# Optimization experiments

Hardware: AMD Instinct MI355X
Metric: run time of the kernel (lower is better)

The kernel has to match this reference:

```python
import jax, jax.numpy as jnp
import numpy as np

B, D, CTX, H = 8192, 64, 256, 512  # batch, latent dim (made.nin), context dim, MADE hidden


def _masks(D, H):
    """Standard MADE natural-ordering masks (Germain et al. 2015)."""
    m0 = np.arange(1, D + 1)                 # input degrees 1..D
    mh = (np.arange(H) % (D - 1)) + 1        # hidden degrees 1..D-1
    M1 = (mh[:, None] >= m0[None, :]).astype(np.float32)   # (H, D)
    M2 = (mh[:, None] >= mh[None, :]).astype(np.float32)   # (H, H)
    mo = np.concatenate([m0, m0])            # outputs = [means; pre_scales]
    Mo = (mo[:, None] > mh[None, :]).astype(np.float32)    # (2D, H)
    return jnp.asarray(M1), jnp.asarray(M2), jnp.asarray(Mo)


def setup_inputs() -> dict:
    key = jax.random.key(0)
    ks = jax.random.split(key, 7)
    s = 0.05
    return {
        "context": jax.random.normal(ks[0], (B, CTX), jnp.float32),
        "eps": jax.random.normal(ks[1], (B, D), jnp.float32),  # reparameterization noise
        "W1": jax.random.normal(ks[2], (H, D), jnp.float32) * s,
        "b1": jnp.zeros((H,), jnp.float32),
        "Wc": jax.random.normal(ks[3], (H, CTX), jnp.float32) * s,
        "W2": jax.random.normal(ks[4], (H, H), jnp.float32) * s,
        "b2": jnp.zeros((H,), jnp.float32),
        "Wo": jax.random.normal(ks[5], (2 * D, H), jnp.float32) * s,
        "bo": jnp.zeros((2 * D,), jnp.float32),
    }


def reference(context, eps, W1, b1, Wc, W2, b2, Wo, bo):
    """AutoRegressiveDistribution.rsample (gaussian): D sequential MADE forwards,
    each extracting column i of (mu, softplus(pre_scale)) and sampling z_i."""
    M1, M2, Mo = _masks(D, H)
    W1m, W2m, Wom = (W1 * M1).T, (W2 * M2).T, (Wo * Mo).T
    ctx_h = context @ Wc.T  # context projection is constant across steps

    def step(z, i):
        h = jax.nn.relu(z @ W1m + ctx_h + b1)   # (B, H)
        h = jax.nn.relu(h @ W2m + b2)           # (B, H)
        out = h @ Wom + bo                      # (B, 2D): [means | pre_scales]
        mu_i = out[:, i]
        scale_i = jax.nn.softplus(out[:, D + i])
        z_i = mu_i + scale_i * eps[:, i]        # Normal(mu, scale).rsample()
        z = z.at[:, i].set(z_i)
        return z, (mu_i, scale_i)

    z0 = jnp.zeros((context.shape[0], D), context.dtype)
    z, (mus, scales) = jax.lax.scan(step, z0, jnp.arange(D))
    # state = (z_sample, mu_inferred, scale_inferred), each (B, D)
    return z, mus.T, scales.T
```

## Files before the change

kernel.cpp:

```cpp
#include <hip/hip_runtime.h>
#include <math.h>


typedef float f2 __attribute__((ext_vector_type(2)));

#define Bn 8192
#define Dn 64
#define CTXn 256
#define Hn 512
#define On 128
#define Rn 8

#define WQ_SZ  (64 * 512 * 12)
#define WOQ_SZ (64 * 64 * 20)
#define WCP_SZ (CTXn * Hn)

__device__ __forceinline__ int perm_of(int p, int* degout) {
  int k, t;
  if (p < 72) { k = p / 9 + 1; t = p - (k - 1) * 9; }
  else        { int pp = p - 72; k = pp / 8 + 9; t = pp - (k - 9) * 8; }
  *degout = k;
  return (k - 1) + 63 * t;
}
__device__ __forceinline__ int inv_perm(int h) {
  int i = h % 63;
  int t = h / 63;
  int base = (i < 9) ? 9 * i : 72 + 8 * (i - 8);
  return base + t;
}

#define R0e 262144
#define R1e (R0e + 32768)
#define R2e (R1e + 65536)
#define R3e (R2e + 131072)
#define R4e (R3e + 35840)
#define R5e (R4e + 1024)
__global__ void prep_kernel(const float* __restrict__ W1, const float* __restrict__ Wc,
                            const float* __restrict__ W2, const float* __restrict__ Wo,
                            const float* __restrict__ b1, const float* __restrict__ b2,
                            float* __restrict__ Wq, float* __restrict__ Woq,
                            float* __restrict__ WcpT, float* __restrict__ b1p,
                            float* __restrict__ b2p) {
  int idx = blockIdx.x * 256 + threadIdx.x;
  if (idx < R0e) {
    int hq = idx >> 9, hp = idx & 511;
    int i = hp % 63, e = hp / 63;
    Wq[i * 6144 + inv_perm(hq) * 12 + e] = W2[idx];
  } else if (idx < R1e) {
    int jj = idx - R0e;
    int hq = jj >> 6, i = jj & 63;
    Wq[i * 6144 + inv_perm(hq) * 12 + 9] = W1[jj];
  } else if (idx < R2e) {
    int jj = idx - R1e;
    int o = jj >> 9, hp = jj & 511;
    int i = hp % 63, p = hp / 63;
    int j = o & 63, half = o >> 6;
    Woq[i * 1280 + j * 20 + half * 10 + p] = Wo[jj];
  } else if (idx < R3e) {
    int jj = idx - R2e;
    int hq = jj >> 8, cc = jj & 255;
    WcpT[cc * 512 + inv_perm(hq)] = Wc[jj];
  } else if (idx < R4e) {
    int z = idx - R3e;
    if (z < 28672) {
      int i = 8 + (z >> 9), q = z & 511;
      Wq[i * 6144 + q * 12 + 8] = 0.f;
    } else {
      int z2 = z - 28672;
      int i = 8 + (z2 >> 7), r = z2 & 127;
      int j = r & 63, half = r >> 6;
      Woq[i * 1280 + j * 20 + half * 10 + 8] = 0.f;
    }
  } else if (idx < R5e) {
    int z = idx - R4e;
    if (z < 512) {
      int dq; int hq = perm_of(z, &dq);
      b1p[z] = b1[hq];
    } else {
      int q = z - 512;
      int dq; int hq = perm_of(q, &dq);
      b2p[q] = b2[hq];
    }
  }
}

__global__ __launch_bounds__(256, 4)
void made_pk_kernel(
    const float* __restrict__ context, const float* __restrict__ WcpT,
    const float* __restrict__ b1p,
    const float* __restrict__ Wq, const float* __restrict__ Woq,
    const float* __restrict__ b2p, const float* __restrict__ bo,
    const float* __restrict__ eps, float* __restrict__ out) {
  __shared__ __align__(16) float ctxR[8][264];
  __shared__ __align__(16) float zcur[8];
  __shared__ __align__(16) float h1g[9][8];
  __shared__ __align__(16) float h2g[9][8];

  int t = threadIdx.x;
  int b0 = blockIdx.x * Rn;
  int rp = t >> 6, l = t & 63;
  int q0 = t, q1 = t + 256;

  int g0 = ((q0 < 72) ? q0 / 9 + 1 : (q0 - 72) / 8 + 9) - 1;
  int g1 = ((q1 - 72) / 8 + 9) - 1;
  int qm = t | 63;
  int gm0s = __builtin_amdgcn_readfirstlane(
      ((qm < 72) ? qm / 9 + 1 : (qm - 72) / 8 + 9) - 1);
  int gm1s = __builtin_amdgcn_readfirstlane(((qm + 256 - 72) / 8 + 9) - 1);

  #pragma unroll
  for (int r = 0; r < 8; ++r)
    ctxR[r][t] = context[(b0 + r) * CTXn + t];
  __syncthreads();

  float acc0[8], acc1[8];
  {
    float bias0 = b1p[q0], bias1 = b1p[q1];
    #pragma unroll
    for (int r = 0; r < 8; ++r) { acc0[r] = bias0; acc1[r] = bias1; }
  }
  {
    const float* wc = WcpT;
    #pragma clang loop unroll(disable)
    for (int c4 = 0; c4 < CTXn / 4; ++c4) {
      float xr[8][4];
      #pragma unroll
      for (int r = 0; r < 8; ++r) {
        float4 x = *(const float4*)&ctxR[r][4 * c4];
        xr[r][0] = x.x; xr[r][1] = x.y; xr[r][2] = x.z; xr[r][3] = x.w;
      }
      #pragma unroll
      for (int k = 0; k < 4; ++k) {
        float w0 = wc[q0], w1 = wc[q1];
        #pragma unroll
        for (int r = 0; r < 8; ++r) {
          acc0[r] = fmaf(xr[r][k], w0, acc0[r]);
          acc1[r] = fmaf(xr[r][k], w1, acc1[r]);
        }
        wc += Hn;
      }
    }
  }

  f2 a10[4], a11[4], a20[4], a21[4];
  #pragma unroll
  for (int r2 = 0; r2 < 4; ++r2) {
    a10[r2] = (f2){acc0[2 * r2], acc0[2 * r2 + 1]};
    a11[r2] = (f2){acc1[2 * r2], acc1[2 * r2 + 1]};
  }
  {
    float bb0 = b2p[q0], bb1 = b2p[q1];
    #pragma unroll
    for (int r2 = 0; r2 < 4; ++r2) {
      a20[r2] = (f2){bb0, bb0};
      a21[r2] = (f2){bb1, bb1};
    }
  }
  f2 ocA = (f2){bo[l], bo[l]};
  f2 ocB = (f2){bo[l + 64], bo[l + 64]};
  f2 ez2 = (f2){eps[(b0 + 2 * rp) * Dn + l], eps[(b0 + 2 * rp + 1) * Dn + l]};
  f2 zs = (f2){0.f, 0.f}, mus = zs, scs = zs;

  const float* wq0p = Wq + (size_t)q0 * 12;
  const float* wq1p = Wq + (size_t)q1 * 12;
  const float* wopp = Woq + (size_t)l * 20;

  #pragma clang loop unroll(disable)
  for (int i = 0; i < Dn; ++i) {
    if (l == i) {
      f2 pre = ocB;
      float sx = fmaxf(pre.x, 0.f) + __logf(1.f + __expf(-fabsf(pre.x)));
      float sy = fmaxf(pre.y, 0.f) + __logf(1.f + __expf(-fabsf(pre.y)));
      f2 sc = (f2){sx, sy};
      f2 z = ocA + sc * ez2;
      *(f2*)&zcur[2 * rp] = z;
      zs = z; mus = ocA; scs = sc;
    }
    __syncthreads();

    int sb = (i < 8) ? 9 * i : 8 * i + 8;
    bool liveB = (i <= gm1s);
    bool liveA = (i <= gm0s);
    float4 A1c0, A1c1, A1c2, A0c0, A0c1, A0c2;
    if (liveB) {
      const float4* a4 = (const float4*)wq1p;
      A1c0 = a4[0]; A1c1 = a4[1]; A1c2 = a4[2];
      if (liveA) {
        const float4* b4 = (const float4*)wq0p;
        A0c0 = b4[0]; A0c1 = b4[1]; A0c2 = b4[2];
      }
      float4 za = *(const float4*)&zcur[0];
      float4 zb = *(const float4*)&zcur[4];
      f2 zc0 = (f2){za.x, za.y}, zc1 = (f2){za.z, za.w};
      f2 zc2 = (f2){zb.x, zb.y}, zc3 = (f2){zb.z, zb.w};
      {
        f2 wv = (f2){A1c2.y, A1c2.y};
        a11[0] += wv * zc0; a11[1] += wv * zc1;
        a11[2] += wv * zc2; a11[3] += wv * zc3;
        if (g1 == i) {
          int pp = q1 - sb;
          float4 h0 = {fmaxf(a11[0].x, 0.f), fmaxf(a11[0].y, 0.f),
                       fmaxf(a11[1].x, 0.f), fmaxf(a11[1].y, 0.f)};
          float4 h1_ = {fmaxf(a11[2].x, 0.f), fmaxf(a11[2].y, 0.f),
                        fmaxf(a11[3].x, 0.f), fmaxf(a11[3].y, 0.f)};
          *(float4*)&h1g[pp][0] = h0; *(float4*)&h1g[pp][4] = h1_;
        }
      }
      if (liveA) {
        f2 wv = (f2){A0c2.y, A0c2.y};
        a10[0] += wv * zc0; a10[1] += wv * zc1;
        a10[2] += wv * zc2; a10[3] += wv * zc3;
        if (g0 == i) {
          int pp = q0 - sb;
          float4 h0 = {fmaxf(a10[0].x, 0.f), fmaxf(a10[0].y, 0.f),
                       fmaxf(a10[1].x, 0.f), fmaxf(a10[1].y, 0.f)};
          float4 h1_ = {fmaxf(a10[2].x, 0.f), fmaxf(a10[2].y, 0.f),
                        fmaxf(a10[3].x, 0.f), fmaxf(a10[3].y, 0.f)};
          *(float4*)&h1g[pp][0] = h0; *(float4*)&h1g[pp][4] = h1_;
        }
      }
    }
    __syncthreads();

    const float4* w4 = (const float4*)wopp;
    float4 B0 = w4[0], B1 = w4[1], B2 = w4[2], B3 = w4[3], B4 = w4[4];

    if (liveB) {
      float wA1[9] = {A1c0.x, A1c0.y, A1c0.z, A1c0.w,
                      A1c1.x, A1c1.y, A1c1.z, A1c1.w, A1c2.x};
      if (liveA) {
        float wA0[9] = {A0c0.x, A0c0.y, A0c0.z, A0c0.w,
                        A0c1.x, A0c1.y, A0c1.z, A0c1.w, A0c2.x};
        #pragma unroll
        for (int p = 0; p < 9; ++p) {
          float4 ha = *(const float4*)&h1g[p][0];
          float4 hb = *(const float4*)&h1g[p][4];
          f2 h0 = (f2){ha.x, ha.y}, h1_ = (f2){ha.z, ha.w};
          f2 h2_ = (f2){hb.x, hb.y}, h3 = (f2){hb.z, hb.w};
          f2 wv1 = (f2){wA1[p], wA1[p]};
          f2 wv0 = (f2){wA0[p], wA0[p]};
          a21[0] += wv1 * h0; a21[1] += wv1 * h1_;
          a21[2] += wv1 * h2_; a21[3] += wv1 * h3;
          a20[0] += wv0 * h0; a20[1] += wv0 * h1_;
          a20[2] += wv0 * h2_; a20[3] += wv0 * h3;
        }
      } else {
        #pragma unroll
        for (int p = 0; p < 9; ++p) {
          float4 ha = *(const float4*)&h1g[p][0];
          float4 hb = *(const float4*)&h1g[p][4];
          f2 h0 = (f2){ha.x, ha.y}, h1_ = (f2){ha.z, ha.w};
          f2 h2_ = (f2){hb.x, hb.y}, h3 = (f2){hb.z, hb.w};
          f2 wv1 = (f2){wA1[p], wA1[p]};
          a21[0] += wv1 * h0; a21[1] += wv1 * h1_;
          a21[2] += wv1 * h2_; a21[3] += wv1 * h3;
        }
      }
      if (g1 == i) {
        int pp = q1 - sb;
        float4 h0 = {fmaxf(a21[0].x, 0.f), fmaxf(a21[0].y, 0.f),
                     fmaxf(a21[1].x, 0.f), fmaxf(a21[1].y, 0.f)};
        float4 h1_ = {fmaxf(a21[2].x, 0.f), fmaxf(a21[2].y, 0.f),
                      fmaxf(a21[3].x, 0.f), fmaxf(a21[3].y, 0.f)};
        *(float4*)&h2g[pp][0] = h0; *(float4*)&h2g[pp][4] = h1_;
      }
      if (liveA && g0 == i) {
        int pp = q0 - sb;
        float4 h0 = {fmaxf(a20[0].x, 0.f), fmaxf(a20[0].y, 0.f),
                     fmaxf(a20[1].x, 0.f), fmaxf(a20[1].y, 0.f)};
        float4 h1_ = {fmaxf(a20[2].x, 0.f), fmaxf(a20[2].y, 0.f),
                      fmaxf(a20[3].x, 0.f), fmaxf(a20[3].y, 0.f)};
        *(float4*)&h2g[pp][0] = h0; *(float4*)&h2g[pp][4] = h1_;
      }
    }
    __syncthreads();

    {
      float wBa[9] = {B0.x, B0.y, B0.z, B0.w, B1.x, B1.y, B1.z, B1.w, B2.x};
      float wBb[9] = {B2.z, B2.w, B3.x, B3.y, B3.z, B3.w, B4.x, B4.y, B4.z};
      #pragma unroll
      for (int p = 0; p < 9; ++p) {
        f2 h = *(const f2*)&h2g[p][2 * rp];
        ocA += (f2){wBa[p], wBa[p]} * h;
        ocB += (f2){wBb[p], wBb[p]} * h;
      }
    }
    wq0p += 6144; wq1p += 6144; wopp += 1280;
  }

  out[(b0 + 2 * rp) * Dn + l] = zs.x;
  out[(b0 + 2 * rp + 1) * Dn + l] = zs.y;
  out[Bn * Dn + (b0 + 2 * rp) * Dn + l] = mus.x;
  out[Bn * Dn + (b0 + 2 * rp + 1) * Dn + l] = mus.y;
  out[2 * Bn * Dn + (b0 + 2 * rp) * Dn + l] = scs.x;
  out[2 * Bn * Dn + (b0 + 2 * rp + 1) * Dn + l] = scs.y;
}

extern "C" void kernel_launch(void* const* d_in, const int* in_sizes, int n_in,
                              void* d_out, int out_size, void* d_ws, size_t ws_size,
                              hipStream_t stream) {
  const float* context = (const float*)d_in[0];
  const float* eps     = (const float*)d_in[1];
  const float* W1      = (const float*)d_in[2];
  const float* b1      = (const float*)d_in[3];
  const float* Wc      = (const float*)d_in[4];
  const float* W2      = (const float*)d_in[5];
  const float* b2      = (const float*)d_in[6];
  const float* Wo      = (const float*)d_in[7];
  const float* bo      = (const float*)d_in[8];
  float* out = (float*)d_out;

  float* ws   = (float*)d_ws;
  float* Wq   = ws;
  float* Woq  = Wq + WQ_SZ;
  float* WcpT = Woq + WOQ_SZ;
  float* b1p  = WcpT + WCP_SZ;
  float* b2p  = b1p + 512;

  prep_kernel<<<(R5e + 255) / 256, 256, 0, stream>>>(
      W1, Wc, W2, Wo, b1, b2, Wq, Woq, WcpT, b1p, b2p);
  made_pk_kernel<<<Bn / Rn, 256, 0, stream>>>(context, WcpT, b1p, Wq, Woq,
                                              b2p, bo, eps, out);
}
```

Before: 240.4 us.

## Prefetch next-step MADE weights, pack context projection as f2, use lightweight barriers

Software-pipelines the per-step W1/W2 weight loads by fetching step i+1's packed weights during step i, hiding global-load latency behind compute. The context-projection weights are interleaved so each thread loads a contiguous f2 pair and uses packed f2 FMAs. __syncthreads is replaced with a barrier that waits only on LDS counters, so outstanding global prefetches are not drained at each barrier. The prefetch registers raise VGPR pressure, and the custom barrier relies on no global-memory ordering being needed across it.

```diff
diff --git a/kernel.cpp b/kernel.cpp
--- a/kernel.cpp
+++ b/kernel.cpp
@@ -14,6 +14,12 @@
 #define WQ_SZ  (64 * 512 * 12)
 #define WOQ_SZ (64 * 64 * 20)
 #define WCP_SZ (CTXn * Hn)
+
+#define BARRIER() do {                                      \
+    asm volatile("s_waitcnt lgkmcnt(0)" ::: "memory");      \
+    __builtin_amdgcn_s_barrier();                           \
+    asm volatile("" ::: "memory");                          \
+  } while (0)
 
 __device__ __forceinline__ int perm_of(int p, int* degout) {
   int k, t;
@@ -59,7 +65,9 @@
   } else if (idx < R3e) {
     int jj = idx - R2e;
     int hq = jj >> 8, cc = jj & 255;
-    WcpT[cc * 512 + inv_perm(hq)] = Wc[jj];
+    int p = inv_perm(hq);
+    int slot = (p < 256) ? (2 * p) : (2 * (p - 256) + 1);
+    WcpT[cc * 512 + slot] = Wc[jj];
   } else if (idx < R4e) {
     int z = idx - R3e;
     if (z < 28672) {
@@ -111,33 +119,32 @@
   #pragma unroll
   for (int r = 0; r < 8; ++r)
     ctxR[r][t] = context[(b0 + r) * CTXn + t];
-  __syncthreads();
-
-  float acc0[8], acc1[8];
+  BARRIER();
+
+  f2 accu[8];
   {
-    float bias0 = b1p[q0], bias1 = b1p[q1];
+    f2 bias = (f2){b1p[q0], b1p[q1]};
     #pragma unroll
-    for (int r = 0; r < 8; ++r) { acc0[r] = bias0; acc1[r] = bias1; }
+    for (int r = 0; r < 8; ++r) accu[r] = bias;
   }
   {
-    const float* wc = WcpT;
+    const float* wc = WcpT + 2 * t;
     #pragma clang loop unroll(disable)
     for (int c4 = 0; c4 < CTXn / 4; ++c4) {
-      float xr[8][4];
+      float4 xr4[8];
       #pragma unroll
-      for (int r = 0; r < 8; ++r) {
-        float4 x = *(const float4*)&ctxR[r][4 * c4];
-        xr[r][0] = x.x; xr[r][1] = x.y; xr[r][2] = x.z; xr[r][3] = x.w;
-      }
+      for (int r = 0; r < 8; ++r)
+        xr4[r] = *(const float4*)&ctxR[r][4 * c4];
       #pragma unroll
       for (int k = 0; k < 4; ++k) {
-        float w0 = wc[q0], w1 = wc[q1];
+        f2 wv = *(const f2*)wc;
+        wc += Hn;
         #pragma unroll
         for (int r = 0; r < 8; ++r) {
-          acc0[r] = fmaf(xr[r][k], w0, acc0[r]);
-          acc1[r] = fmaf(xr[r][k], w1, acc1[r]);
-        }
-        wc += Hn;
+          float xk = (k == 0) ? xr4[r].x : (k == 1) ? xr4[r].y
+                   : (k == 2) ? xr4[r].z : xr4[r].w;
+          accu[r] += (f2){xk, xk} * wv;
+        }
       }
     }
   }
@@ -145,8 +152,8 @@
   f2 a10[4], a11[4], a20[4], a21[4];
   #pragma unroll
   for (int r2 = 0; r2 < 4; ++r2) {
-    a10[r2] = (f2){acc0[2 * r2], acc0[2 * r2 + 1]};
-    a11[r2] = (f2){acc1[2 * r2], acc1[2 * r2 + 1]};
+    a10[r2] = (f2){accu[2 * r2].x, accu[2 * r2 + 1].x};
+    a11[r2] = (f2){accu[2 * r2].y, accu[2 * r2 + 1].y};
   }
   {
     float bb0 = b2p[q0], bb1 = b2p[q1];
@@ -164,6 +171,15 @@
   const float* wq0p = Wq + (size_t)q0 * 12;
   const float* wq1p = Wq + (size_t)q1 * 12;
   const float* wopp = Woq + (size_t)l * 20;
+
+  float4 A1c0, A1c1, A1c2, A0c0, A0c1, A0c2;
+  {
+    const float4* a4 = (const float4*)wq1p;
+    A1c0 = a4[0]; A1c1 = a4[1]; A1c2 = a4[2];
+    const float4* b4 = (const float4*)wq0p;
+    A0c0 = b4[0]; A0c1 = b4[1]; A0c2 = b4[2];
+    wq0p += 6144; wq1p += 6144;
+  }
 
   #pragma clang loop unroll(disable)
   for (int i = 0; i < Dn; ++i) {
@@ -176,19 +192,24 @@
       *(f2*)&zcur[2 * rp] = z;
       zs = z; mus = ocA; scs = sc;
     }
-    __syncthreads();
+    BARRIER();
+
+    bool nliveB = (i + 1 <= gm1s);
+    bool nliveA = (i + 1 <= gm0s);
+    float4 P1c0, P1c1, P1c2, P0c0, P0c1, P0c2;
+    if (nliveB) {
+      const float4* a4 = (const float4*)wq1p;
+      P1c0 = a4[0]; P1c1 = a4[1]; P1c2 = a4[2];
+      if (nliveA) {
+        const float4* b4 = (const float4*)wq0p;
+        P0c0 = b4[0]; P0c1 = b4[1]; P0c2 = b4[2];
+      }
+    }
 
     int sb = (i < 8) ? 9 * i : 8 * i + 8;
     bool liveB = (i <= gm1s);
     bool liveA = (i <= gm0s);
-    float4 A1c0, A1c1, A1c2, A0c0, A0c1, A0c2;
     if (liveB) {
-      const float4* a4 = (const float4*)wq1p;
-      A1c0 = a4[0]; A1c1 = a4[1]; A1c2 = a4[2];
-      if (liveA) {
-        const float4* b4 = (const float4*)wq0p;
-        A0c0 = b4[0]; A0c1 = b4[1]; A0c2 = b4[2];
-      }
       float4 za = *(const float4*)&zcur[0];
       float4 zb = *(const float4*)&zcur[4];
       f2 zc0 = (f2){za.x, za.y}, zc1 = (f2){za.z, za.w};
@@ -220,7 +241,7 @@
         }
       }
     }
-    __syncthreads();
+    BARRIER();
 
     const float4* w4 = (const float4*)wopp;
     float4 B0 = w4[0], B1 = w4[1], B2 = w4[2], B3 = w4[3], B4 = w4[4];
@@ -273,7 +294,7 @@
         *(float4*)&h2g[pp][0] = h0; *(float4*)&h2g[pp][4] = h1_;
       }
     }
-    __syncthreads();
+    BARRIER();
 
     {
       float wBa[9] = {B0.x, B0.y, B0.z, B0.w, B1.x, B1.y, B1.z, B1.w, B2.x};
@@ -284,6 +305,11 @@
         ocA += (f2){wBa[p], wBa[p]} * h;
         ocB += (f2){wBb[p], wBb[p]} * h;
       }
+    }
+
+    if (nliveB) {
+      A1c0 = P1c0; A1c1 = P1c1; A1c2 = P1c2;
+      if (nliveA) { A0c0 = P0c0; A0c1 = P0c1; A0c2 = P0c2; }
     }
     wq0p += 6144; wq1p += 6144; wopp += 1280;
   }
```

Result: slower. 431.4 us (+79.5%).
